# Kernel optimization log

Hardware: AMD Instinct MI355X
Metric: run time of the kernel (lower is better)

The kernel has to match this reference:

```python
import jax, jax.numpy as jnp
import numpy as np

N_NODES = 10000
N_EDGES = 640000
D_FEAT = 128
HID = 64


def setup_inputs() -> dict:
    key = jax.random.key(0)
    k1, k2, k3, k4 = jax.random.split(key, 4)
    x = jax.random.normal(k1, (N_NODES, D_FEAT), dtype=jnp.float32)
    indices = jax.random.randint(k2, (2, N_EDGES), 0, N_NODES, dtype=jnp.int64)
    # Kaiming-ish small init for the tiny MLP
    W1 = jax.random.normal(k3, (D_FEAT, HID), dtype=jnp.float32) / np.sqrt(D_FEAT)
    b1 = jnp.zeros((HID,), dtype=jnp.float32)
    W2 = jax.random.normal(k4, (HID, 1), dtype=jnp.float32) / np.sqrt(HID)
    b2 = jnp.zeros((1,), dtype=jnp.float32)
    return {"x": x, "indices": indices, "W1": W1, "b1": b1, "W2": W2, "b2": b2}


def reference(x, indices, W1, b1, W2, b2):
    # Gather endpoint features per edge, abs diff: [nnz, d]
    x_diff = jnp.abs(x[indices[0]] - x[indices[1]])
    # 2-layer MLP with ReLU then Sigmoid -> per-edge scalar (new sparse values)
    h = jax.nn.relu(x_diff @ W1 + b1)          # [nnz, hid]
    data = jax.nn.sigmoid(h @ W2 + b2)[:, 0]   # [nnz]
    return data
```

## Files before the change

### kernel.cpp

```cpp
#include <hip/hip_runtime.h>


#define DF 128
#define HID 64
#define AST 136

typedef _Float16 half8   __attribute__((ext_vector_type(8)));
typedef _Float16 half4_t __attribute__((ext_vector_type(4)));
typedef float    floatx4 __attribute__((ext_vector_type(4)));

__device__ __forceinline__ float sigmoidf_(float t) {
    return __builtin_amdgcn_rcpf(1.0f + __expf(-t));
}

__global__ void cvt_pre(const float* __restrict__ x, const float* __restrict__ W1,
                        _Float16* __restrict__ xh, _Float16* __restrict__ w1t, int n4)
{
    const int i = blockIdx.x * blockDim.x + threadIdx.x;
    if (i < n4) {
        float4 v = ((const float4*)x)[i];
        half4_t h = { (_Float16)v.x, (_Float16)v.y, (_Float16)v.z, (_Float16)v.w };
        ((half4_t*)xh)[i] = h;
    }
    if (i < DF * HID) {
        const int h = i >> 7, f = i & 127;
        w1t[i] = (_Float16)W1[f * HID + h];
    }
}

#define ROW(idv) *(const half8*)(xh + (size_t)(idv) * DF + goff)

#define ISSUE(S, D, sIv, dIv)                                   \
    S##0 = ROW((sIv).x); S##1 = ROW((sIv).y);                   \
    S##2 = ROW((sIv).z); S##3 = ROW((sIv).w);                   \
    D##0 = ROW((dIv).x); D##1 = ROW((dIv).y);                   \
    D##2 = ROW((dIv).z); D##3 = ROW((dIv).w);

#define PROC(t, S, D) {                                                        \
    union { half8 h; uint4 u; } U0, U1, U2, U3;                                \
    U0.h = S##0 - D##0; U1.h = S##1 - D##1;                                    \
    U2.h = S##2 - D##2; U3.h = S##3 - D##3;                                    \
    U0.u.x &= 0x7FFF7FFFu; U0.u.y &= 0x7FFF7FFFu;                              \
    U0.u.z &= 0x7FFF7FFFu; U0.u.w &= 0x7FFF7FFFu;                              \
    U1.u.x &= 0x7FFF7FFFu; U1.u.y &= 0x7FFF7FFFu;                              \
    U1.u.z &= 0x7FFF7FFFu; U1.u.w &= 0x7FFF7FFFu;                              \
    U2.u.x &= 0x7FFF7FFFu; U2.u.y &= 0x7FFF7FFFu;                              \
    U2.u.z &= 0x7FFF7FFFu; U2.u.w &= 0x7FFF7FFFu;                              \
    U3.u.x &= 0x7FFF7FFFu; U3.u.y &= 0x7FFF7FFFu;                              \
    U3.u.z &= 0x7FFF7FFFu; U3.u.w &= 0x7FFF7FFFu;                              \
    *(half8*)(ldsw + ((t) * 16 + q * 4 + 0) * AST + goff) = U0.h;              \
    *(half8*)(ldsw + ((t) * 16 + q * 4 + 1) * AST + goff) = U1.h;              \
    *(half8*)(ldsw + ((t) * 16 + q * 4 + 2) * AST + goff) = U2.h;              \
    *(half8*)(ldsw + ((t) * 16 + q * 4 + 3) * AST + goff) = U3.h; }

__global__ __launch_bounds__(256, 2) void edge_mlp_v9(
    const _Float16* __restrict__ xh, const _Float16* __restrict__ w1t,
    const int* __restrict__ idx,
    const float* __restrict__ b1, const float* __restrict__ W2,
    const float* __restrict__ b2,
    float* __restrict__ out, int n_edges, int ngroups, int gstride)
{
    __shared__ __attribute__((aligned(16))) _Float16 lds_d[4][64 * AST];

    const int tid = threadIdx.x;
    const int L   = tid & 63;
    const int r16 = L & 15;
    const int q   = L >> 4;
    const int wv  = tid >> 6;
    _Float16* const ldsw = &lds_d[wv][0];

    half8 wf[4][4];
#pragma unroll
    for (int mt = 0; mt < 4; ++mt)
#pragma unroll
        for (int kb = 0; kb < 4; ++kb)
            wf[mt][kb] = *(const half8*)(w1t + (size_t)(mt * 16 + r16) * DF + kb * 32 + q * 8);
#pragma unroll
    for (int mt = 0; mt < 4; ++mt)
#pragma unroll
        for (int kb = 0; kb < 4; ++kb)
            asm volatile("" : "+v"(wf[mt][kb]));

    half4_t b1h[4], w2h[4];
#pragma unroll
    for (int mt = 0; mt < 4; ++mt)
#pragma unroll
        for (int r = 0; r < 4; ++r) {
            b1h[mt][r] = (_Float16)b1[mt * 16 + q * 4 + r];
            w2h[mt][r] = (_Float16)W2[mt * 16 + q * 4 + r];
        }
    const float b2v = b2[0];

    const int goff = r16 * 8;
    const int idof = q * 4;

    const int g0 = blockIdx.x;

    int4 sI0, sI1, sI2, sI3, dI0, dI1, dI2, dI3;
    {
        const int eb = g0 * 256 + wv * 64;
        sI0 = *(const int4*)(idx + eb +  0 + idof);
        sI1 = *(const int4*)(idx + eb + 16 + idof);
        sI2 = *(const int4*)(idx + eb + 32 + idof);
        sI3 = *(const int4*)(idx + eb + 48 + idof);
        dI0 = *(const int4*)(idx + n_edges + eb +  0 + idof);
        dI1 = *(const int4*)(idx + n_edges + eb + 16 + idof);
        dI2 = *(const int4*)(idx + n_edges + eb + 32 + idof);
        dI3 = *(const int4*)(idx + n_edges + eb + 48 + idof);
    }

#pragma unroll 1
    for (int g = g0; g < ngroups; g += gstride) {
        half8 sa0, sa1, sa2, sa3, da0, da1, da2, da3;
        half8 sb0, sb1, sb2, sb3, db0, db1, db2, db3;

        ISSUE(sa, da, sI0, dI0);
        ISSUE(sb, db, sI1, dI1);
        PROC(0, sa, da);
        ISSUE(sa, da, sI2, dI2);
        PROC(1, sb, db);
        ISSUE(sb, db, sI3, dI3);
        PROC(2, sa, da);

        int4 sN0, sN1, sN2, sN3, dN0, dN1, dN2, dN3;
        {
            int gn = g + gstride; if (gn >= ngroups) gn = g;
            const int ebn = gn * 256 + wv * 64;
            sN0 = *(const int4*)(idx + ebn +  0 + idof);
            sN1 = *(const int4*)(idx + ebn + 16 + idof);
            sN2 = *(const int4*)(idx + ebn + 32 + idof);
            sN3 = *(const int4*)(idx + ebn + 48 + idof);
            dN0 = *(const int4*)(idx + n_edges + ebn +  0 + idof);
            dN1 = *(const int4*)(idx + n_edges + ebn + 16 + idof);
            dN2 = *(const int4*)(idx + n_edges + ebn + 32 + idof);
            dN3 = *(const int4*)(idx + n_edges + ebn + 48 + idof);
        }

        PROC(3, sb, db);

        floatx4 acc[4][4];
#pragma unroll
        for (int mt = 0; mt < 4; ++mt)
#pragma unroll
            for (int et = 0; et < 4; ++et)
                acc[mt][et] = (floatx4){0.f, 0.f, 0.f, 0.f};
#pragma unroll
        for (int kb = 0; kb < 4; ++kb) {
#pragma unroll
            for (int et = 0; et < 4; ++et) {
                const half8 bf = *(const half8*)(ldsw + (et * 16 + r16) * AST + kb * 32 + q * 8);
                acc[0][et] = __builtin_amdgcn_mfma_f32_16x16x32_f16(wf[0][kb], bf, acc[0][et], 0, 0, 0);
                acc[1][et] = __builtin_amdgcn_mfma_f32_16x16x32_f16(wf[1][kb], bf, acc[1][et], 0, 0, 0);
                acc[2][et] = __builtin_amdgcn_mfma_f32_16x16x32_f16(wf[2][kb], bf, acc[2][et], 0, 0, 0);
                acc[3][et] = __builtin_amdgcn_mfma_f32_16x16x32_f16(wf[3][kb], bf, acc[3][et], 0, 0, 0);
            }
        }

        sI0 = sN0; sI1 = sN1; sI2 = sN2; sI3 = sN3;
        dI0 = dN0; dI1 = dN1; dI2 = dN2; dI3 = dN3;

#pragma unroll
        for (int et = 0; et < 4; ++et) {
            float part = 0.f;
#pragma unroll
            for (int mt = 0; mt < 4; ++mt)
#pragma unroll
                for (int r = 0; r < 4; ++r)
                    part = fmaf(fmaxf(acc[mt][et][r] + (float)b1h[mt][r], 0.f),
                                (float)w2h[mt][r], part);
            part += __shfl_xor(part, 16, 64);
            part += __shfl_xor(part, 32, 64);
            if (L < 16)
                out[g * 256 + wv * 64 + et * 16 + L] = sigmoidf_(part + b2v);
        }
    }
}

__global__ void edge_naive(const float* __restrict__ x, const int* __restrict__ idx,
                           const float* __restrict__ W1, const float* __restrict__ b1,
                           const float* __restrict__ W2, const float* __restrict__ b2,
                           float* __restrict__ out, int n_edges, int start)
{
    int e = start + blockIdx.x * blockDim.x + threadIdx.x;
    if (e >= n_edges) return;
    int s = idx[e], d = idx[n_edges + e];
    float t = b2[0];
    for (int j = 0; j < HID; ++j) {
        float h = b1[j];
        for (int k = 0; k < DF; ++k)
            h = fmaf(fabsf(x[(size_t)s * DF + k] - x[(size_t)d * DF + k]), W1[(size_t)k * HID + j], h);
        t = fmaf(fmaxf(h, 0.f), W2[j], t);
    }
    out[e] = sigmoidf_(t);
}

extern "C" void kernel_launch(void* const* d_in, const int* in_sizes, int n_in,
                              void* d_out, int out_size, void* d_ws, size_t ws_size,
                              hipStream_t stream) {
    const float* x   = (const float*)d_in[0];
    const int*   idx = (const int*)d_in[1];
    const float* W1  = (const float*)d_in[2];
    const float* b1  = (const float*)d_in[3];
    const float* W2  = (const float*)d_in[4];
    const float* b2  = (const float*)d_in[5];
    float* out = (float*)d_out;

    const int n_edges = in_sizes[1] / 2;
    const int n_x     = in_sizes[0];
    const int ngroups = n_edges / 256;
    const int rem     = n_edges - ngroups * 256;

    const size_t xh_bytes  = ((size_t)n_x * sizeof(_Float16) + 255) & ~(size_t)255;
    const size_t w1t_bytes = (size_t)DF * HID * sizeof(_Float16);
    const bool ok = (ws_size >= xh_bytes + w1t_bytes) && (n_x % 4 == 0);

    if (ok && ngroups > 0) {
        _Float16* xh  = (_Float16*)d_ws;
        _Float16* w1t = (_Float16*)((char*)d_ws + xh_bytes);
        const int n4 = n_x / 4;
        cvt_pre<<<(n4 + 255) / 256, 256, 0, stream>>>(x, W1, xh, w1t, n4);

        const int grid = ngroups < 512 ? ngroups : 512;
        edge_mlp_v9<<<grid, 256, 0, stream>>>(xh, w1t, idx, b1, W2, b2,
                                              out, n_edges, ngroups, grid);
        if (rem > 0)
            edge_naive<<<(rem + 63) / 64, 64, 0, stream>>>(x, idx, W1, b1, W2, b2,
                                                           out, n_edges, ngroups * 256);
    } else {
        edge_naive<<<(n_edges + 63) / 64, 64, 0, stream>>>(x, idx, W1, b1, W2, b2,
                                                           out, n_edges, 0);
    }
}
```

Before: 95.45 us.

## Split hidden dimension across waves with block-level LDS reduction and idx prefetch

Each block now handles 64 edges, and each wave computes one 16-wide slice of the hidden layer rather than all 64 hidden units for its own 64 edges. Per-wave partial sums go through a double-buffered LDS array and are reduced one iteration later. This cuts per-wave registers and LDS so four blocks can share a CU, and the grid doubles to 1024. The preprocessing kernel also reads the whole index array once to warm the cache. The cost is a __syncthreads per iteration and the cross-wave reduction.

```diff
diff --git a/kernel.cpp b/kernel.cpp
--- a/kernel.cpp
+++ b/kernel.cpp
@@ -6,7 +6,6 @@
 #define AST 136
 
 typedef _Float16 half8   __attribute__((ext_vector_type(8)));
-typedef _Float16 half4_t __attribute__((ext_vector_type(4)));
 typedef float    floatx4 __attribute__((ext_vector_type(4)));
 
 __device__ __forceinline__ float sigmoidf_(float t) {
@@ -14,165 +13,153 @@
 }
 
 __global__ void cvt_pre(const float* __restrict__ x, const float* __restrict__ W1,
-                        _Float16* __restrict__ xh, _Float16* __restrict__ w1t, int n4)
+                        const int* __restrict__ idx,
+                        _Float16* __restrict__ xh, _Float16* __restrict__ w1t,
+                        int n4, int ni4)
 {
     const int i = blockIdx.x * blockDim.x + threadIdx.x;
     if (i < n4) {
         float4 v = ((const float4*)x)[i];
-        half4_t h = { (_Float16)v.x, (_Float16)v.y, (_Float16)v.z, (_Float16)v.w };
-        ((half4_t*)xh)[i] = h;
+        union { _Float16 h[4]; ushort2 u2[2]; } hh;
+        hh.h[0] = (_Float16)v.x; hh.h[1] = (_Float16)v.y;
+        hh.h[2] = (_Float16)v.z; hh.h[3] = (_Float16)v.w;
+        *(uint2*)(xh + (size_t)i * 4) = *(uint2*)&hh;
     }
     if (i < DF * HID) {
         const int h = i >> 7, f = i & 127;
         w1t[i] = (_Float16)W1[f * HID + h];
     }
+    if (i < ni4) {
+        int4 t = ((const int4*)idx)[i];
+        asm volatile("" :: "v"(t.x), "v"(t.y), "v"(t.z), "v"(t.w));
+    }
 }
 
 #define ROW(idv) *(const half8*)(xh + (size_t)(idv) * DF + goff)
 
-#define ISSUE(S, D, sIv, dIv)                                   \
-    S##0 = ROW((sIv).x); S##1 = ROW((sIv).y);                   \
-    S##2 = ROW((sIv).z); S##3 = ROW((sIv).w);                   \
-    D##0 = ROW((dIv).x); D##1 = ROW((dIv).y);                   \
-    D##2 = ROW((dIv).z); D##3 = ROW((dIv).w);
-
-#define PROC(t, S, D) {                                                        \
-    union { half8 h; uint4 u; } U0, U1, U2, U3;                                \
-    U0.h = S##0 - D##0; U1.h = S##1 - D##1;                                    \
-    U2.h = S##2 - D##2; U3.h = S##3 - D##3;                                    \
-    U0.u.x &= 0x7FFF7FFFu; U0.u.y &= 0x7FFF7FFFu;                              \
-    U0.u.z &= 0x7FFF7FFFu; U0.u.w &= 0x7FFF7FFFu;                              \
-    U1.u.x &= 0x7FFF7FFFu; U1.u.y &= 0x7FFF7FFFu;                              \
-    U1.u.z &= 0x7FFF7FFFu; U1.u.w &= 0x7FFF7FFFu;                              \
-    U2.u.x &= 0x7FFF7FFFu; U2.u.y &= 0x7FFF7FFFu;                              \
-    U2.u.z &= 0x7FFF7FFFu; U2.u.w &= 0x7FFF7FFFu;                              \
-    U3.u.x &= 0x7FFF7FFFu; U3.u.y &= 0x7FFF7FFFu;                              \
-    U3.u.z &= 0x7FFF7FFFu; U3.u.w &= 0x7FFF7FFFu;                              \
-    *(half8*)(ldsw + ((t) * 16 + q * 4 + 0) * AST + goff) = U0.h;              \
-    *(half8*)(ldsw + ((t) * 16 + q * 4 + 1) * AST + goff) = U1.h;              \
-    *(half8*)(ldsw + ((t) * 16 + q * 4 + 2) * AST + goff) = U2.h;              \
-    *(half8*)(ldsw + ((t) * 16 + q * 4 + 3) * AST + goff) = U3.h; }
-
-__global__ __launch_bounds__(256, 2) void edge_mlp_v9(
+__global__ __launch_bounds__(256, 4) void edge_mlp_v12(
     const _Float16* __restrict__ xh, const _Float16* __restrict__ w1t,
     const int* __restrict__ idx,
     const float* __restrict__ b1, const float* __restrict__ W2,
     const float* __restrict__ b2,
     float* __restrict__ out, int n_edges, int ngroups, int gstride)
 {
-    __shared__ __attribute__((aligned(16))) _Float16 lds_d[4][64 * AST];
+    __shared__ __attribute__((aligned(16))) _Float16 lds_d[2][64 * AST];
+    __shared__ float lds_p[2][4][64];
 
     const int tid = threadIdx.x;
     const int L   = tid & 63;
     const int r16 = L & 15;
     const int q   = L >> 4;
     const int wv  = tid >> 6;
-    _Float16* const ldsw = &lds_d[wv][0];
-
-    half8 wf[4][4];
-#pragma unroll
-    for (int mt = 0; mt < 4; ++mt)
-#pragma unroll
-        for (int kb = 0; kb < 4; ++kb)
-            wf[mt][kb] = *(const half8*)(w1t + (size_t)(mt * 16 + r16) * DF + kb * 32 + q * 8);
-#pragma unroll
-    for (int mt = 0; mt < 4; ++mt)
-#pragma unroll
-        for (int kb = 0; kb < 4; ++kb)
-            asm volatile("" : "+v"(wf[mt][kb]));
-
-    half4_t b1h[4], w2h[4];
-#pragma unroll
-    for (int mt = 0; mt < 4; ++mt)
-#pragma unroll
-        for (int r = 0; r < 4; ++r) {
-            b1h[mt][r] = (_Float16)b1[mt * 16 + q * 4 + r];
-            w2h[mt][r] = (_Float16)W2[mt * 16 + q * 4 + r];
-        }
+
+    half8 wf[4];
+#pragma unroll
+    for (int kb = 0; kb < 4; ++kb)
+        wf[kb] = *(const half8*)(w1t + (size_t)(wv * 16 + r16) * DF + kb * 32 + q * 8);
+
+    float b1v[4], w2v[4];
+#pragma unroll
+    for (int r = 0; r < 4; ++r) {
+        b1v[r] = b1[wv * 16 + q * 4 + r];
+        w2v[r] = W2[wv * 16 + q * 4 + r];
+    }
     const float b2v = b2[0];
 
     const int goff = r16 * 8;
-    const int idof = q * 4;
+    const int eoff = wv * 16 + q * 4;
 
     const int g0 = blockIdx.x;
 
-    int4 sI0, sI1, sI2, sI3, dI0, dI1, dI2, dI3;
+    int4 sI, dI, sN, dN;
+    sI = *(const int4*)(idx + g0 * 64 + eoff);
+    dI = *(const int4*)(idx + n_edges + g0 * 64 + eoff);
+
+    half8 s0, s1, s2, s3, d0, d1, d2, d3;
+    s0 = ROW(sI.x); s1 = ROW(sI.y); s2 = ROW(sI.z); s3 = ROW(sI.w);
+    d0 = ROW(dI.x); d1 = ROW(dI.y); d2 = ROW(dI.z); d3 = ROW(dI.w);
+
     {
-        const int eb = g0 * 256 + wv * 64;
-        sI0 = *(const int4*)(idx + eb +  0 + idof);
-        sI1 = *(const int4*)(idx + eb + 16 + idof);
-        sI2 = *(const int4*)(idx + eb + 32 + idof);
-        sI3 = *(const int4*)(idx + eb + 48 + idof);
-        dI0 = *(const int4*)(idx + n_edges + eb +  0 + idof);
-        dI1 = *(const int4*)(idx + n_edges + eb + 16 + idof);
-        dI2 = *(const int4*)(idx + n_edges + eb + 32 + idof);
-        dI3 = *(const int4*)(idx + n_edges + eb + 48 + idof);
-    }
-
+        int gn = g0 + gstride; if (gn >= ngroups) gn = g0;
+        sI = *(const int4*)(idx + gn * 64 + eoff);
+        dI = *(const int4*)(idx + n_edges + gn * 64 + eoff);
+    }
+
+    int it = 0, gprev = 0;
 #pragma unroll 1
-    for (int g = g0; g < ngroups; g += gstride) {
-        half8 sa0, sa1, sa2, sa3, da0, da1, da2, da3;
-        half8 sb0, sb1, sb2, sb3, db0, db1, db2, db3;
-
-        ISSUE(sa, da, sI0, dI0);
-        ISSUE(sb, db, sI1, dI1);
-        PROC(0, sa, da);
-        ISSUE(sa, da, sI2, dI2);
-        PROC(1, sb, db);
-        ISSUE(sb, db, sI3, dI3);
-        PROC(2, sa, da);
-
-        int4 sN0, sN1, sN2, sN3, dN0, dN1, dN2, dN3;
+    for (int g = g0; g < ngroups; g += gstride, ++it) {
+        _Float16* const bufw = &lds_d[it & 1][0];
+
         {
-            int gn = g + gstride; if (gn >= ngroups) gn = g;
-            const int ebn = gn * 256 + wv * 64;
-            sN0 = *(const int4*)(idx + ebn +  0 + idof);
-            sN1 = *(const int4*)(idx + ebn + 16 + idof);
-            sN2 = *(const int4*)(idx + ebn + 32 + idof);
-            sN3 = *(const int4*)(idx + ebn + 48 + idof);
-            dN0 = *(const int4*)(idx + n_edges + ebn +  0 + idof);
-            dN1 = *(const int4*)(idx + n_edges + ebn + 16 + idof);
-            dN2 = *(const int4*)(idx + n_edges + ebn + 32 + idof);
-            dN3 = *(const int4*)(idx + n_edges + ebn + 48 + idof);
-        }
-
-        PROC(3, sb, db);
-
-        floatx4 acc[4][4];
-#pragma unroll
-        for (int mt = 0; mt < 4; ++mt)
-#pragma unroll
-            for (int et = 0; et < 4; ++et)
-                acc[mt][et] = (floatx4){0.f, 0.f, 0.f, 0.f};
+            union { half8 h; uint4 u; } U0, U1, U2, U3;
+            U0.h = s0 - d0; U1.h = s1 - d1; U2.h = s2 - d2; U3.h = s3 - d3;
+            U0.u.x &= 0x7FFF7FFFu; U0.u.y &= 0x7FFF7FFFu;
+            U0.u.z &= 0x7FFF7FFFu; U0.u.w &= 0x7FFF7FFFu;
+            U1.u.x &= 0x7FFF7FFFu; U1.u.y &= 0x7FFF7FFFu;
+            U1.u.z &= 0x7FFF7FFFu; U1.u.w &= 0x7FFF7FFFu;
+            U2.u.x &= 0x7FFF7FFFu; U2.u.y &= 0x7FFF7FFFu;
+            U2.u.z &= 0x7FFF7FFFu; U2.u.w &= 0x7FFF7FFFu;
+            U3.u.x &= 0x7FFF7FFFu; U3.u.y &= 0x7FFF7FFFu;
+            U3.u.z &= 0x7FFF7FFFu; U3.u.w &= 0x7FFF7FFFu;
+            *(half8*)(bufw + (eoff + 0) * AST + goff) = U0.h;
+            *(half8*)(bufw + (eoff + 1) * AST + goff) = U1.h;
+            *(half8*)(bufw + (eoff + 2) * AST + goff) = U2.h;
+            *(half8*)(bufw + (eoff + 3) * AST + goff) = U3.h;
+        }
+
+        {
+            int gn = g + 2 * gstride; if (gn >= ngroups) gn = g;
+            sN = *(const int4*)(idx + gn * 64 + eoff);
+            dN = *(const int4*)(idx + n_edges + gn * 64 + eoff);
+        }
+
+        s0 = ROW(sI.x); s1 = ROW(sI.y); s2 = ROW(sI.z); s3 = ROW(sI.w);
+        d0 = ROW(dI.x); d1 = ROW(dI.y); d2 = ROW(dI.z); d3 = ROW(dI.w);
+
+        __syncthreads();
+
+        floatx4 acc[4];
+#pragma unroll
+        for (int et = 0; et < 4; ++et)
+            acc[et] = (floatx4){0.f, 0.f, 0.f, 0.f};
 #pragma unroll
         for (int kb = 0; kb < 4; ++kb) {
 #pragma unroll
             for (int et = 0; et < 4; ++et) {
-                const half8 bf = *(const half8*)(ldsw + (et * 16 + r16) * AST + kb * 32 + q * 8);
-                acc[0][et] = __builtin_amdgcn_mfma_f32_16x16x32_f16(wf[0][kb], bf, acc[0][et], 0, 0, 0);
-                acc[1][et] = __builtin_amdgcn_mfma_f32_16x16x32_f16(wf[1][kb], bf, acc[1][et], 0, 0, 0);
-                acc[2][et] = __builtin_amdgcn_mfma_f32_16x16x32_f16(wf[2][kb], bf, acc[2][et], 0, 0, 0);
-                acc[3][et] = __builtin_amdgcn_mfma_f32_16x16x32_f16(wf[3][kb], bf, acc[3][et], 0, 0, 0);
+                const half8 bf = *(const half8*)(bufw + (et * 16 + r16) * AST + kb * 32 + q * 8);
+                acc[et] = __builtin_amdgcn_mfma_f32_16x16x32_f16(wf[kb], bf, acc[et], 0, 0, 0);
             }
         }
 
-        sI0 = sN0; sI1 = sN1; sI2 = sN2; sI3 = sN3;
-        dI0 = dN0; dI1 = dN1; dI2 = dN2; dI3 = dN3;
-
+        float* const pp = &lds_p[it & 1][wv][0];
 #pragma unroll
         for (int et = 0; et < 4; ++et) {
-            float part = 0.f;
-#pragma unroll
-            for (int mt = 0; mt < 4; ++mt)
-#pragma unroll
-                for (int r = 0; r < 4; ++r)
-                    part = fmaf(fmaxf(acc[mt][et][r] + (float)b1h[mt][r], 0.f),
-                                (float)w2h[mt][r], part);
-            part += __shfl_xor(part, 16, 64);
-            part += __shfl_xor(part, 32, 64);
-            if (L < 16)
-                out[g * 256 + wv * 64 + et * 16 + L] = sigmoidf_(part + b2v);
-        }
+            float p = 0.f;
+#pragma unroll
+            for (int r = 0; r < 4; ++r)
+                p = fmaf(fmaxf(acc[et][r] + b1v[r], 0.f), w2v[r], p);
+            p += __shfl_xor(p, 16, 64);
+            p += __shfl_xor(p, 32, 64);
+            if (L < 16) pp[et * 16 + L] = p;
+        }
+
+        if (it > 0 && L < 16) {
+            const float* const pq = &lds_p[(it & 1) ^ 1][0][0];
+            const int e = wv * 16 + L;
+            float v = pq[0 * 64 + e] + pq[1 * 64 + e] + pq[2 * 64 + e] + pq[3 * 64 + e];
+            out[gprev * 64 + e] = sigmoidf_(v + b2v);
+        }
+
+        gprev = g;
+        sI = sN; dI = dN;
+    }
+
+    __syncthreads();
+    if (it > 0 && L < 16) {
+        const float* const pq = &lds_p[(it & 1) ^ 1][0][0];
+        const int e = wv * 16 + L;
+        float v = pq[0 * 64 + e] + pq[1 * 64 + e] + pq[2 * 64 + e] + pq[3 * 64 + e];
+        out[gprev * 64 + e] = sigmoidf_(v + b2v);
     }
 }
 
@@ -207,8 +194,8 @@
 
     const int n_edges = in_sizes[1] / 2;
     const int n_x     = in_sizes[0];
-    const int ngroups = n_edges / 256;
-    const int rem     = n_edges - ngroups * 256;
+    const int ngroups = n_edges / 64;
+    const int rem     = n_edges - ngroups * 64;
 
     const size_t xh_bytes  = ((size_t)n_x * sizeof(_Float16) + 255) & ~(size_t)255;
     const size_t w1t_bytes = (size_t)DF * HID * sizeof(_Float16);
@@ -217,15 +204,17 @@
     if (ok && ngroups > 0) {
         _Float16* xh  = (_Float16*)d_ws;
         _Float16* w1t = (_Float16*)((char*)d_ws + xh_bytes);
-        const int n4 = n_x / 4;
-        cvt_pre<<<(n4 + 255) / 256, 256, 0, stream>>>(x, W1, xh, w1t, n4);
-
-        const int grid = ngroups < 512 ? ngroups : 512;
-        edge_mlp_v9<<<grid, 256, 0, stream>>>(xh, w1t, idx, b1, W2, b2,
-                                              out, n_edges, ngroups, grid);
+        const int n4  = n_x / 4;
+        const int ni4 = (n_edges * 2) / 4;
+        const int pgrid = (n4 > ni4 ? n4 : ni4);
+        cvt_pre<<<(pgrid + 255) / 256, 256, 0, stream>>>(x, W1, idx, xh, w1t, n4, ni4);
+
+        const int grid = ngroups < 1024 ? ngroups : 1024;
+        edge_mlp_v12<<<grid, 256, 0, stream>>>(xh, w1t, idx, b1, W2, b2,
+                                               out, n_edges, ngroups, grid);
         if (rem > 0)
             edge_naive<<<(rem + 63) / 64, 64, 0, stream>>>(x, idx, W1, b1, W2, b2,
-                                                           out, n_edges, ngroups * 256);
+                                                           out, n_edges, ngroups * 64);
     } else {
         edge_naive<<<(n_edges + 63) / 64, 64, 0, stream>>>(x, idx, W1, b1, W2, b2,
                                                            out, n_edges, 0);
```

Measured after the change: 97.16 us. No clear change (+1.8%).

## Load gathered rows directly into MFMA B-fragments, dropping the LDS staging

Applied to the files above, without the earlier changes.

Each lane now gathers the features for its own edge, strided so they land directly in the MFMA B-operand layout. This removes the LDS write/read round trip and the 4x64x136 shared buffer. It also drops software prefetch of next-group indices, loads indices once per wave and shuffles them, and raises occupancy (launch bounds 3, grid 768). In exchange there is less memory-level parallelism per wave, because each 16-edge tile loads and computes serially without the previous double-buffering, and the loads become narrower per row.

```diff
diff --git a/kernel.cpp b/kernel.cpp
--- a/kernel.cpp
+++ b/kernel.cpp
@@ -3,7 +3,6 @@
 
 #define DF 128
 #define HID 64
-#define AST 136
 
 typedef _Float16 half8   __attribute__((ext_vector_type(8)));
 typedef _Float16 half4_t __attribute__((ext_vector_type(4)));
@@ -28,46 +27,18 @@
     }
 }
 
-#define ROW(idv) *(const half8*)(xh + (size_t)(idv) * DF + goff)
-
-#define ISSUE(S, D, sIv, dIv)                                   \
-    S##0 = ROW((sIv).x); S##1 = ROW((sIv).y);                   \
-    S##2 = ROW((sIv).z); S##3 = ROW((sIv).w);                   \
-    D##0 = ROW((dIv).x); D##1 = ROW((dIv).y);                   \
-    D##2 = ROW((dIv).z); D##3 = ROW((dIv).w);
-
-#define PROC(t, S, D) {                                                        \
-    union { half8 h; uint4 u; } U0, U1, U2, U3;                                \
-    U0.h = S##0 - D##0; U1.h = S##1 - D##1;                                    \
-    U2.h = S##2 - D##2; U3.h = S##3 - D##3;                                    \
-    U0.u.x &= 0x7FFF7FFFu; U0.u.y &= 0x7FFF7FFFu;                              \
-    U0.u.z &= 0x7FFF7FFFu; U0.u.w &= 0x7FFF7FFFu;                              \
-    U1.u.x &= 0x7FFF7FFFu; U1.u.y &= 0x7FFF7FFFu;                              \
-    U1.u.z &= 0x7FFF7FFFu; U1.u.w &= 0x7FFF7FFFu;                              \
-    U2.u.x &= 0x7FFF7FFFu; U2.u.y &= 0x7FFF7FFFu;                              \
-    U2.u.z &= 0x7FFF7FFFu; U2.u.w &= 0x7FFF7FFFu;                              \
-    U3.u.x &= 0x7FFF7FFFu; U3.u.y &= 0x7FFF7FFFu;                              \
-    U3.u.z &= 0x7FFF7FFFu; U3.u.w &= 0x7FFF7FFFu;                              \
-    *(half8*)(ldsw + ((t) * 16 + q * 4 + 0) * AST + goff) = U0.h;              \
-    *(half8*)(ldsw + ((t) * 16 + q * 4 + 1) * AST + goff) = U1.h;              \
-    *(half8*)(ldsw + ((t) * 16 + q * 4 + 2) * AST + goff) = U2.h;              \
-    *(half8*)(ldsw + ((t) * 16 + q * 4 + 3) * AST + goff) = U3.h; }
-
-__global__ __launch_bounds__(256, 2) void edge_mlp_v9(
+__global__ __launch_bounds__(256, 3) void edge_mlp_v15(
     const _Float16* __restrict__ xh, const _Float16* __restrict__ w1t,
     const int* __restrict__ idx,
     const float* __restrict__ b1, const float* __restrict__ W2,
     const float* __restrict__ b2,
     float* __restrict__ out, int n_edges, int ngroups, int gstride)
 {
-    __shared__ __attribute__((aligned(16))) _Float16 lds_d[4][64 * AST];
-
     const int tid = threadIdx.x;
     const int L   = tid & 63;
     const int r16 = L & 15;
     const int q   = L >> 4;
     const int wv  = tid >> 6;
-    _Float16* const ldsw = &lds_d[wv][0];
 
     half8 wf[4][4];
 #pragma unroll
@@ -91,87 +62,65 @@
         }
     const float b2v = b2[0];
 
-    const int goff = r16 * 8;
-    const int idof = q * 4;
-
     const int g0 = blockIdx.x;
-
-    int4 sI0, sI1, sI2, sI3, dI0, dI1, dI2, dI3;
-    {
-        const int eb = g0 * 256 + wv * 64;
-        sI0 = *(const int4*)(idx + eb +  0 + idof);
-        sI1 = *(const int4*)(idx + eb + 16 + idof);
-        sI2 = *(const int4*)(idx + eb + 32 + idof);
-        sI3 = *(const int4*)(idx + eb + 48 + idof);
-        dI0 = *(const int4*)(idx + n_edges + eb +  0 + idof);
-        dI1 = *(const int4*)(idx + n_edges + eb + 16 + idof);
-        dI2 = *(const int4*)(idx + n_edges + eb + 32 + idof);
-        dI3 = *(const int4*)(idx + n_edges + eb + 48 + idof);
-    }
 
 #pragma unroll 1
     for (int g = g0; g < ngroups; g += gstride) {
-        half8 sa0, sa1, sa2, sa3, da0, da1, da2, da3;
-        half8 sb0, sb1, sb2, sb3, db0, db1, db2, db3;
+        const int ebase = g * 256 + wv * 64;
 
-        ISSUE(sa, da, sI0, dI0);
-        ISSUE(sb, db, sI1, dI1);
-        PROC(0, sa, da);
-        ISSUE(sa, da, sI2, dI2);
-        PROC(1, sb, db);
-        ISSUE(sb, db, sI3, dI3);
-        PROC(2, sa, da);
-
-        int4 sN0, sN1, sN2, sN3, dN0, dN1, dN2, dN3;
-        {
-            int gn = g + gstride; if (gn >= ngroups) gn = g;
-            const int ebn = gn * 256 + wv * 64;
-            sN0 = *(const int4*)(idx + ebn +  0 + idof);
-            sN1 = *(const int4*)(idx + ebn + 16 + idof);
-            sN2 = *(const int4*)(idx + ebn + 32 + idof);
-            sN3 = *(const int4*)(idx + ebn + 48 + idof);
-            dN0 = *(const int4*)(idx + n_edges + ebn +  0 + idof);
-            dN1 = *(const int4*)(idx + n_edges + ebn + 16 + idof);
-            dN2 = *(const int4*)(idx + n_edges + ebn + 32 + idof);
-            dN3 = *(const int4*)(idx + n_edges + ebn + 48 + idof);
-        }
-
-        PROC(3, sb, db);
-
-        floatx4 acc[4][4];
-#pragma unroll
-        for (int mt = 0; mt < 4; ++mt)
-#pragma unroll
-            for (int et = 0; et < 4; ++et)
-                acc[mt][et] = (floatx4){0.f, 0.f, 0.f, 0.f};
-#pragma unroll
-        for (int kb = 0; kb < 4; ++kb) {
-#pragma unroll
-            for (int et = 0; et < 4; ++et) {
-                const half8 bf = *(const half8*)(ldsw + (et * 16 + r16) * AST + kb * 32 + q * 8);
-                acc[0][et] = __builtin_amdgcn_mfma_f32_16x16x32_f16(wf[0][kb], bf, acc[0][et], 0, 0, 0);
-                acc[1][et] = __builtin_amdgcn_mfma_f32_16x16x32_f16(wf[1][kb], bf, acc[1][et], 0, 0, 0);
-                acc[2][et] = __builtin_amdgcn_mfma_f32_16x16x32_f16(wf[2][kb], bf, acc[2][et], 0, 0, 0);
-                acc[3][et] = __builtin_amdgcn_mfma_f32_16x16x32_f16(wf[3][kb], bf, acc[3][et], 0, 0, 0);
-            }
-        }
-
-        sI0 = sN0; sI1 = sN1; sI2 = sN2; sI3 = sN3;
-        dI0 = dN0; dI1 = dN1; dI2 = dN2; dI3 = dN3;
+        const int sAll = idx[ebase + L];
+        const int dAll = idx[n_edges + ebase + L];
 
 #pragma unroll
-        for (int et = 0; et < 4; ++et) {
+        for (int bt = 0; bt < 4; ++bt) {
+            const int se = __shfl(sAll, bt * 16 + r16, 64);
+            const int de = __shfl(dAll, bt * 16 + r16, 64);
+            const _Float16* sp = xh + (size_t)se * DF + q * 8;
+            const _Float16* dp = xh + (size_t)de * DF + q * 8;
+
+            half8 s0 = *(const half8*)(sp +  0);
+            half8 s1 = *(const half8*)(sp + 32);
+            half8 s2 = *(const half8*)(sp + 64);
+            half8 s3 = *(const half8*)(sp + 96);
+            half8 d0 = *(const half8*)(dp +  0);
+            half8 d1 = *(const half8*)(dp + 32);
+            half8 d2 = *(const half8*)(dp + 64);
+            half8 d3 = *(const half8*)(dp + 96);
+
+            union { half8 h; uint4 u; } B0, B1, B2, B3;
+            B0.h = s0 - d0; B1.h = s1 - d1; B2.h = s2 - d2; B3.h = s3 - d3;
+            B0.u.x &= 0x7FFF7FFFu; B0.u.y &= 0x7FFF7FFFu;
+            B0.u.z &= 0x7FFF7FFFu; B0.u.w &= 0x7FFF7FFFu;
+            B1.u.x &= 0x7FFF7FFFu; B1.u.y &= 0x7FFF7FFFu;
+            B1.u.z &= 0x7FFF7FFFu; B1.u.w &= 0x7FFF7FFFu;
+            B2.u.x &= 0x7FFF7FFFu; B2.u.y &= 0x7FFF7FFFu;
+            B2.u.z &= 0x7FFF7FFFu; B2.u.w &= 0x7FFF7FFFu;
+            B3.u.x &= 0x7FFF7FFFu; B3.u.y &= 0x7FFF7FFFu;
+            B3.u.z &= 0x7FFF7FFFu; B3.u.w &= 0x7FFF7FFFu;
+
+            floatx4 acc[4];
+#pragma unroll
+            for (int mt = 0; mt < 4; ++mt)
+                acc[mt] = (floatx4){0.f, 0.f, 0.f, 0.f};
+#pragma unroll
+            for (int mt = 0; mt < 4; ++mt) {
+                acc[mt] = __builtin_amdgcn_mfma_f32_16x16x32_f16(wf[mt][0], B0.h, acc[mt], 0, 0, 0);
+                acc[mt] = __builtin_amdgcn_mfma_f32_16x16x32_f16(wf[mt][1], B1.h, acc[mt], 0, 0, 0);
+                acc[mt] = __builtin_amdgcn_mfma_f32_16x16x32_f16(wf[mt][2], B2.h, acc[mt], 0, 0, 0);
+                acc[mt] = __builtin_amdgcn_mfma_f32_16x16x32_f16(wf[mt][3], B3.h, acc[mt], 0, 0, 0);
+            }
+
             float part = 0.f;
 #pragma unroll
             for (int mt = 0; mt < 4; ++mt)
 #pragma unroll
                 for (int r = 0; r < 4; ++r)
-                    part = fmaf(fmaxf(acc[mt][et][r] + (float)b1h[mt][r], 0.f),
+                    part = fmaf(fmaxf(acc[mt][r] + (float)b1h[mt][r], 0.f),
                                 (float)w2h[mt][r], part);
             part += __shfl_xor(part, 16, 64);
             part += __shfl_xor(part, 32, 64);
             if (L < 16)
-                out[g * 256 + wv * 64 + et * 16 + L] = sigmoidf_(part + b2v);
+                out[ebase + bt * 16 + L] = sigmoidf_(part + b2v);
         }
     }
 }
@@ -220,9 +169,9 @@
         const int n4 = n_x / 4;
         cvt_pre<<<(n4 + 255) / 256, 256, 0, stream>>>(x, W1, xh, w1t, n4);
 
-        const int grid = ngroups < 512 ? ngroups : 512;
-        edge_mlp_v9<<<grid, 256, 0, stream>>>(xh, w1t, idx, b1, W2, b2,
-                                              out, n_edges, ngroups, grid);
+        const int grid = ngroups < 768 ? ngroups : 768;
+        edge_mlp_v15<<<grid, 256, 0, stream>>>(xh, w1t, idx, b1, W2, b2,
+                                               out, n_edges, ngroups, grid);
         if (rem > 0)
             edge_naive<<<(rem + 63) / 64, 64, 0, stream>>>(x, idx, W1, b1, W2, b2,
                                                            out, n_edges, ngroups * 256);
```

Measured after the change: 113.2 us. 18.6% more time.
